# Performance work log

Measured on AMD Instinct MI355X. Metric: run time of the kernel, lower is better.

## Reference

```python
import jax, jax.numpy as jnp
import numpy as np


def _make_grid(H, W):
    # Matches tf.meshgrid default 'xy' indexing: x varies along columns.
    x_t = jnp.linspace(-1.0, 1.0, W)
    y_t = jnp.linspace(-1.0, 1.0, H)
    xx, yy = jnp.meshgrid(x_t, y_t)  # each [H, W]
    return jnp.stack([xx.ravel(), yy.ravel(), jnp.ones(H * W, jnp.float32)], axis=0)  # [3, H*W]


def setup_inputs() -> dict:
    key = jax.random.key(0)
    k1, k2 = jax.random.split(key)
    stimuli = jax.random.normal(k1, (4, 32, 304, 608, 1), dtype=jnp.float32)
    eye = jax.random.normal(k2, (4, 32, 2, 3), dtype=jnp.float32)
    return {"stimuli": stimuli, "eye": eye}


def reference(stimuli, eye):
    B, T, H, W, C = stimuli.shape
    N = B * T
    HW = H * W
    img = stimuli.reshape(N, HW, C).astype(jnp.float32)   # flattened per-frame image
    aff = eye.reshape(N, 2, 3).astype(jnp.float32)        # 2x3 affine per frame

    grid = _make_grid(H, W)                               # [3, HW]
    T_g = jnp.einsum('nij,jk->nik', aff, grid)            # [N, 2, HW]
    x = (T_g[:, 0] + 1.0) * (W / 2.0)                     # [N, HW] source x in pixels
    y = (T_g[:, 1] + 1.0) * (H / 2.0)

    x0 = jnp.floor(x).astype(jnp.int32)
    y0 = jnp.floor(y).astype(jnp.int32)
    x1 = x0 + 1
    y1 = y0 + 1
    x0 = jnp.clip(x0, 0, W - 1)
    x1 = jnp.clip(x1, 0, W - 1)
    y0 = jnp.clip(y0, 0, H - 1)
    y1 = jnp.clip(y1, 0, H - 1)

    def gather(yy, xx):
        idx = yy * W + xx                                  # [N, HW]
        return jnp.take_along_axis(img, idx[..., None], axis=1)  # [N, HW, C]

    Ia = gather(y0, x0)
    Ib = gather(y1, x0)
    Ic = gather(y0, x1)
    Id = gather(y1, x1)

    x0f = x0.astype(jnp.float32)
    x1f = x1.astype(jnp.float32)
    y0f = y0.astype(jnp.float32)
    y1f = y1.astype(jnp.float32)
    wa = ((x1f - x) * (y1f - y))[..., None]
    wb = ((x1f - x) * (y - y0f))[..., None]
    wc = ((x - x0f) * (y1f - y))[..., None]
    wd = ((x - x0f) * (y - y0f))[..., None]

    out = wa * Ia + wb * Ib + wc * Ic + wd * Id            # [N, HW, C]
    return out.reshape(B, T, H, W, C)
```

## Files before the change

kernel.cpp:

```cpp
#include <hip/hip_runtime.h>

#define BH 304
#define BW 608
#define BHW (BH * BW)
#define NFRAMES 128

typedef float vf2 __attribute__((ext_vector_type(2)));

__global__ __launch_bounds__(128) void warp_bilinear_lean_kernel(
    const float* __restrict__ stimuli,
    const float* __restrict__ eye,
    float* __restrict__ out)
{
    const int n    = blockIdx.y;
    const int blk  = blockIdx.x;
    const int base = blk * 512;
    const int py0  = base / BW;
    const int pc0  = base - py0 * BW;

    const float* aff = eye + n * 6;
    const float a00 = aff[0], a01 = aff[1], a02 = aff[2];
    const float a10 = aff[3], a11 = aff[4], a12 = aff[5];

    const float yyr0 = -1.0f + 2.0f * (float)py0       / (float)(BH - 1);
    const float yyr1 = -1.0f + 2.0f * (float)(py0 + 1) / (float)(BH - 1);
    const float a01yy0 = a01 * yyr0, a01yy1 = a01 * yyr1;
    const float a11yy0 = a11 * yyr0, a11yy1 = a11 * yyr1;

    const float* __restrict__ img = stimuli + (size_t)n * BHW;

    float fxs[4], fys[4];
    bool  ok[4];
    vf2   vA[4], vB[4];

    #pragma unroll
    for (int k = 0; k < 4; ++k) {
        const int off  = pc0 + (int)threadIdx.x + k * 128;
        const bool wrap = (off >= BW);
        const int px   = wrap ? off - BW : off;
        const float a01yy = wrap ? a01yy1 : a01yy0;
        const float a11yy = wrap ? a11yy1 : a11yy0;

        const float xx = -1.0f + 2.0f * (float)px / (float)(BW - 1);
        const float x = (a00 * xx + a01yy + a02 + 1.0f) * (0.5f * (float)BW);
        const float y = (a10 * xx + a11yy + a12 + 1.0f) * (0.5f * (float)BH);

        const float x0f = floorf(x);
        const float y0f = floorf(y);
        const int x0 = (int)x0f;
        const int y0 = (int)y0f;

        fxs[k] = x - x0f;
        fys[k] = y - y0f;
        ok[k] = ((unsigned)x0 < (unsigned)(BW - 1)) & ((unsigned)y0 < (unsigned)(BH - 1));

        const int xp = min(max(x0, 0), BW - 2);
        const int yp = min(max(y0, 0), BH - 2);
        const float* rowA = img + yp * BW + xp;
        __builtin_memcpy(&vA[k], rowA, 8);
        __builtin_memcpy(&vB[k], rowA + BW, 8);
    }

    #pragma unroll
    for (int k = 0; k < 4; ++k) {
        const float fx = fxs[k], fy = fys[k];
        const float ix0 = vA[k].x + fx * (vA[k].y - vA[k].x);
        const float ix1 = vB[k].x + fx * (vB[k].y - vB[k].x);
        float r = ix0 + fy * (ix1 - ix0);
        r = ok[k] ? r : 0.0f;
        out[(size_t)n * BHW + base + (int)threadIdx.x + k * 128] = r;
    }
}

extern "C" void kernel_launch(void* const* d_in, const int* in_sizes, int n_in,
                              void* d_out, int out_size, void* d_ws, size_t ws_size,
                              hipStream_t stream) {
    const float* stimuli = (const float*)d_in[0];
    const float* eye     = (const float*)d_in[1];
    float* out = (float*)d_out;

    dim3 grid(BHW / 512, NFRAMES);
    dim3 block(128);
    warp_bilinear_lean_kernel<<<grid, block, 0, stream>>>(stimuli, eye, out);
}
```

Measured before the change: 192.3 us.

## Process adjacent pixel pairs per thread sharing a 4x3 source window

Each thread now computes two horizontally adjacent output pixels. When the frame's affine step per pixel is small enough, it loads one shared 4x3 neighbourhood with three 16-byte loads and selects the corners from registers. Frames with large per-pixel steps fall back to the per-pixel gather path. Block size goes to 256 threads with a vectorized 8-byte store; this adds select logic and a divergent fallback branch.

```diff
diff --git a/kernel.cpp b/kernel.cpp
--- a/kernel.cpp
+++ b/kernel.cpp
@@ -6,15 +6,15 @@
 #define NFRAMES 128
 
 typedef float vf2 __attribute__((ext_vector_type(2)));
+typedef float vf4 __attribute__((ext_vector_type(4)));
 
-__global__ __launch_bounds__(128) void warp_bilinear_lean_kernel(
+__global__ __launch_bounds__(256) void warp_bilinear_pair_kernel(
     const float* __restrict__ stimuli,
     const float* __restrict__ eye,
     float* __restrict__ out)
 {
     const int n    = blockIdx.y;
-    const int blk  = blockIdx.x;
-    const int base = blk * 512;
+    const int base = blockIdx.x * 512;
     const int py0  = base / BW;
     const int pc0  = base - py0 * BW;
 
@@ -27,48 +27,103 @@
     const float a01yy0 = a01 * yyr0, a01yy1 = a01 * yyr1;
     const float a11yy0 = a11 * yyr0, a11yy1 = a11 * yyr1;
 
+    const float dxpp = a00 * (float)BW / (float)(BW - 1);
+    const float dypp = a10 * (float)BH / (float)(BW - 1);
+
     const float* __restrict__ img = stimuli + (size_t)n * BHW;
+    const bool fast = (fabsf(dxpp) < 1.98f) && (fabsf(dypp) < 0.999f);
 
-    float fxs[4], fys[4];
-    bool  ok[4];
-    vf2   vA[4], vB[4];
-
-    #pragma unroll
-    for (int k = 0; k < 4; ++k) {
-        const int off  = pc0 + (int)threadIdx.x + k * 128;
-        const bool wrap = (off >= BW);
+    if (fast) {
+        const int off  = pc0 + 2 * (int)threadIdx.x;
+        const bool wrap = off >= BW;
         const int px   = wrap ? off - BW : off;
         const float a01yy = wrap ? a01yy1 : a01yy0;
         const float a11yy = wrap ? a11yy1 : a11yy0;
 
         const float xx = -1.0f + 2.0f * (float)px / (float)(BW - 1);
-        const float x = (a00 * xx + a01yy + a02 + 1.0f) * (0.5f * (float)BW);
-        const float y = (a10 * xx + a11yy + a12 + 1.0f) * (0.5f * (float)BH);
+        const float xe = (a00 * xx + a01yy + a02 + 1.0f) * (0.5f * (float)BW);
+        const float ye = (a10 * xx + a11yy + a12 + 1.0f) * (0.5f * (float)BH);
+        const float xo = xe + dxpp;
+        const float yo = ye + dypp;
 
-        const float x0f = floorf(x);
-        const float y0f = floorf(y);
-        const int x0 = (int)x0f;
-        const int y0 = (int)y0f;
+        const float xef = floorf(xe), xof = floorf(xo);
+        const float yef = floorf(ye), yof = floorf(yo);
+        const int x0e = (int)xef, x0o = (int)xof;
+        const int y0e = (int)yef, y0o = (int)yof;
 
-        fxs[k] = x - x0f;
-        fys[k] = y - y0f;
-        ok[k] = ((unsigned)x0 < (unsigned)(BW - 1)) & ((unsigned)y0 < (unsigned)(BH - 1));
+        const int xm = min(x0e, x0o);
+        const int ym = min(y0e, y0o);
+        const int xp = min(max(xm, 0), BW - 4);
+        const int yp = min(max(ym, 0), BH - 3);
 
-        const int xp = min(max(x0, 0), BW - 2);
-        const int yp = min(max(y0, 0), BH - 2);
-        const float* rowA = img + yp * BW + xp;
-        __builtin_memcpy(&vA[k], rowA, 8);
-        __builtin_memcpy(&vB[k], rowA + BW, 8);
-    }
+        const float* rowp = img + yp * BW + xp;
+        vf4 r0, r1, r2;
+        __builtin_memcpy(&r0, rowp, 16);
+        __builtin_memcpy(&r1, rowp + BW, 16);
+        __builtin_memcpy(&r2, rowp + 2 * BW, 16);
 
-    #pragma unroll
-    for (int k = 0; k < 4; ++k) {
-        const float fx = fxs[k], fy = fys[k];
-        const float ix0 = vA[k].x + fx * (vA[k].y - vA[k].x);
-        const float ix1 = vB[k].x + fx * (vB[k].y - vB[k].x);
-        float r = ix0 + fy * (ix1 - ix0);
-        r = ok[k] ? r : 0.0f;
-        out[(size_t)n * BHW + base + (int)threadIdx.x + k * 128] = r;
+        float res2[2];
+        #pragma unroll
+        for (int k = 0; k < 2; ++k) {
+            const float x   = k ? xo  : xe;
+            const float y   = k ? yo  : ye;
+            const float x0f = k ? xof : xef;
+            const float y0f = k ? yof : yef;
+            const int   x0  = k ? x0o : x0e;
+            const int   y0  = k ? y0o : y0e;
+
+            const int dx = x0 - xp;
+            const int dy = y0 - yp;
+            const vf4 ra = (dy >= 1) ? r1 : r0;
+            const vf4 rb = (dy >= 1) ? r2 : r1;
+            const float Ia = (dx >= 1) ? ((dx >= 2) ? ra.z : ra.y) : ra.x;
+            const float Ic = (dx >= 1) ? ((dx >= 2) ? ra.w : ra.z) : ra.y;
+            const float Ib = (dx >= 1) ? ((dx >= 2) ? rb.z : rb.y) : rb.x;
+            const float Id = (dx >= 1) ? ((dx >= 2) ? rb.w : rb.z) : rb.y;
+
+            const float fx = x - x0f;
+            const float fy = y - y0f;
+            const float ix0 = Ia + fx * (Ic - Ia);
+            const float ix1 = Ib + fx * (Id - Ib);
+            const float r = ix0 + fy * (ix1 - ix0);
+            const bool ok = ((unsigned)x0 < (unsigned)(BW - 1)) &&
+                            ((unsigned)y0 < (unsigned)(BH - 1));
+            res2[k] = ok ? r : 0.0f;
+        }
+
+        vf2 res; res.x = res2[0]; res.y = res2[1];
+        __builtin_memcpy(out + (size_t)n * BHW + base + 2 * (int)threadIdx.x, &res, 8);
+    } else {
+        #pragma unroll
+        for (int k = 0; k < 2; ++k) {
+            const int off2 = pc0 + (int)threadIdx.x + k * 256;
+            const bool w2  = off2 >= BW;
+            const int px2  = w2 ? off2 - BW : off2;
+            const float a01y = w2 ? a01yy1 : a01yy0;
+            const float a11y = w2 ? a11yy1 : a11yy0;
+
+            const float xx2 = -1.0f + 2.0f * (float)px2 / (float)(BW - 1);
+            const float x = (a00 * xx2 + a01y + a02 + 1.0f) * (0.5f * (float)BW);
+            const float y = (a10 * xx2 + a11y + a12 + 1.0f) * (0.5f * (float)BH);
+
+            const float x0f = floorf(x), y0f = floorf(y);
+            const int x0 = (int)x0f, y0 = (int)y0f;
+            const int xq = min(max(x0, 0), BW - 2);
+            const int yq = min(max(y0, 0), BH - 2);
+
+            const float* rp = img + yq * BW + xq;
+            vf2 va, vb;
+            __builtin_memcpy(&va, rp, 8);
+            __builtin_memcpy(&vb, rp + BW, 8);
+
+            const float fx = x - x0f, fy = y - y0f;
+            const bool ok = ((unsigned)x0 < (unsigned)(BW - 1)) &&
+                            ((unsigned)y0 < (unsigned)(BH - 1));
+            const float ix0 = va.x + fx * (va.y - va.x);
+            const float ix1 = vb.x + fx * (vb.y - vb.x);
+            const float r = ix0 + fy * (ix1 - ix0);
+            out[(size_t)n * BHW + base + (int)threadIdx.x + k * 256] = ok ? r : 0.0f;
+        }
     }
 }
 
@@ -80,6 +135,6 @@
     float* out = (float*)d_out;
 
     dim3 grid(BHW / 512, NFRAMES);
-    dim3 block(128);
-    warp_bilinear_lean_kernel<<<grid, block, 0, stream>>>(stimuli, eye, out);
+    dim3 block(256);
+    warp_bilinear_pair_kernel<<<grid, block, 0, stream>>>(stimuli, eye, out);
 }
```

New measurement: 203.8 us. 1.06x slower.
